# Kernel tuning notes

Hardware: AMD Instinct MI355X
Metric: run time of the kernel (lower is better)

## Reference

```python
import jax, jax.numpy as jnp
import numpy as np

B, S, HIDDEN = 4, 2048, 1024
HEADS = 16
D = HIDDEN // HEADS  # att_size = 64
SCALE = D ** -0.5


def setup_inputs() -> dict:
    key = jax.random.key(0)
    k_x, k_qkv, k_out = jax.random.split(key, 3)
    x = jax.random.normal(k_x, (B, S, HIDDEN), dtype=jnp.float32)
    # torch Linear weights: (out_features, in_features); xavier-uniform init
    lim_qkv = np.sqrt(6.0 / (HIDDEN + 3 * HIDDEN))
    W_qkv = jax.random.uniform(k_qkv, (3 * HEADS * D, HIDDEN), dtype=jnp.float32,
                               minval=-lim_qkv, maxval=lim_qkv)
    lim_out = np.sqrt(6.0 / (HIDDEN + HIDDEN))
    W_out = jax.random.uniform(k_out, (HIDDEN, HEADS * D), dtype=jnp.float32,
                               minval=-lim_out, maxval=lim_out)
    return {"x": x, "W_qkv": W_qkv, "W_out": W_out}


def reference(x, W_qkv, W_out):
    b, s, _ = x.shape
    # fused QKV projection; feature layout along output dim is [3][heads][d]
    qkv = jnp.einsum('bsh,fh->bsf', x, W_qkv).reshape(b, s, 3, HEADS, D)
    q = qkv[:, :, 0].transpose(0, 2, 1, 3) * SCALE  # [b, H, s, d]
    k = qkv[:, :, 1].transpose(0, 2, 1, 3)
    v = qkv[:, :, 2].transpose(0, 2, 1, 3)
    scores = jnp.einsum('bhqd,bhkd->bhqk', q, k)
    attn = jax.nn.softmax(scores, axis=-1)
    ctx = jnp.einsum('bhqk,bhkd->bhqd', attn, v)
    ctx = ctx.transpose(0, 2, 1, 3).reshape(b, s, HEADS * D)
    return jnp.einsum('bsf,hf->bsh', ctx, W_out)
```

## Files before the change

### kernel.cpp

```cpp
#include <hip/hip_runtime.h>
#include <hip/hip_bf16.h>
#include <stdint.h>
#include <math.h>


using half8  = __attribute__((ext_vector_type(8))) _Float16;
using half4  = __attribute__((ext_vector_type(4))) _Float16;
using f32x4  = __attribute__((ext_vector_type(4))) float;
using f32x16 = __attribute__((ext_vector_type(16))) float;
using u32x4  = __attribute__((ext_vector_type(4))) unsigned int;

#define HID   1024
#define NHEAD 16
#define HDIM  64
#define NB    4
#define SEQ   2048
#define MROWS (NB*SEQ)
#define NKTH  16

typedef __attribute__((address_space(1))) const void* gas_t;
typedef __attribute__((address_space(3))) void*       las_t;

__global__ void conv_h(const float* __restrict__ in, _Float16* __restrict__ out,
                       int n4, int nscale, float qs){
  int i = blockIdx.x * 256 + threadIdx.x;
  if (i >= n4) return;
  f32x4 v = *(const f32x4*)(in + (size_t)i*4);
  int row = (i*4) >> 10;
  if (row < nscale){ v[0]*=qs; v[1]*=qs; v[2]*=qs; v[3]*=qs; }
  half4 o = { (_Float16)v[0], (_Float16)v[1], (_Float16)v[2], (_Float16)v[3] };
  *(half4*)(out + (size_t)i*4) = o;
}

__device__ __forceinline__ void stage_tile(const _Float16* __restrict__ g,
                                           char* lds, int t, int wid){
#pragma unroll
  for (int i = 0; i < 4; ++i){
    int tl  = i*256 + t;
    int row = tl >> 3;
    int srcb = (((tl & 7) << 4)) ^ ((row & 7) << 4);
    __builtin_amdgcn_global_load_lds(
        (gas_t)((const char*)(g + (size_t)row*1024) + srcb),
        (las_t)(lds + (i*256 + wid*64)*16), 16, 0, 0);
  }
}

template<int EPI>
__global__ __launch_bounds__(256)
void gemmh(const _Float16* __restrict__ A, const _Float16* __restrict__ B,
           float* __restrict__ C,
           _Float16* __restrict__ qo, _Float16* __restrict__ ko,
           _Float16* __restrict__ vo, int N)
{
  __shared__ __align__(16) char lA[128*128];
  __shared__ __align__(16) char lB[128*128];
  int t = threadIdx.x, lane = t & 63, wid = t >> 6;
  int fq = lane >> 4, fr = lane & 15;
  int m0 = blockIdx.x * 128, n0 = blockIdx.y * 128;
  int wm = (wid >> 1) * 64, wn = (wid & 1) * 64;
  f32x4 acc[4][4] = {};

  for (int kt = 0; kt < NKTH; ++kt){
    stage_tile(A + (size_t)m0*1024 + kt*64, lA, t, wid);
    stage_tile(B + (size_t)n0*1024 + kt*64, lB, t, wid);
    __syncthreads();
#pragma unroll
    for (int kc = 0; kc < 2; ++kc){
      half8 af[4], bf[4];
#pragma unroll
      for (int mi = 0; mi < 4; ++mi){
        int row = wm + mi*16 + fr;
        af[mi] = *(const half8*)(lA + row*128 + ((kc*64 + fq*16) ^ ((row&7)<<4)));
      }
#pragma unroll
      for (int ni = 0; ni < 4; ++ni){
        int row = wn + ni*16 + fr;
        bf[ni] = *(const half8*)(lB + row*128 + ((kc*64 + fq*16) ^ ((row&7)<<4)));
      }
      __builtin_amdgcn_s_setprio(1);
#pragma unroll
      for (int mi = 0; mi < 4; ++mi)
#pragma unroll
        for (int ni = 0; ni < 4; ++ni)
          acc[mi][ni] = __builtin_amdgcn_mfma_f32_16x16x32_f16(af[mi], bf[ni],
                                                               acc[mi][ni], 0, 0, 0);
      __builtin_amdgcn_s_setprio(0);
    }
    __syncthreads();
  }

  if (EPI == 0){
#pragma unroll
    for (int mi = 0; mi < 4; ++mi)
#pragma unroll
      for (int ni = 0; ni < 4; ++ni)
#pragma unroll
        for (int r = 0; r < 4; ++r){
          int m = m0 + wm + mi*16 + fq*4 + r;
          int n = n0 + wn + ni*16 + fr;
          C[(size_t)m*N + n] = acc[mi][ni][r];
        }
  } else {
    int cls = n0 >> 10;
#pragma unroll
    for (int mi = 0; mi < 4; ++mi)
#pragma unroll
      for (int ni = 0; ni < 4; ++ni)
#pragma unroll
        for (int r = 0; r < 4; ++r){
          int m = m0 + wm + mi*16 + fq*4 + r;
          int n = n0 + wn + ni*16 + fr;
          float v = acc[mi][ni][r];
          int b = m >> 11, s = m & 2047;
          int nn = n & 1023;
          int h = nn >> 6, d2 = nn & 63;
          int bh = b*NHEAD + h;
          if (cls == 0){
            qo[((size_t)bh*SEQ + s)*HDIM + d2] = (_Float16)v;
          } else if (cls == 1){
            int kb = s >> 5, l31 = s & 31;
            int c = d2 >> 4, hi8 = (d2 >> 3) & 1, e = d2 & 7;
            ko[((((size_t)bh*64 + kb)*4 + c)*64 + hi8*32 + l31)*8 + e] = (_Float16)v;
          } else {
            int kb = s >> 5, kk = s & 31;
            int kh = kk >> 4, hv = (kk >> 3) & 1, e = kk & 7;
            int dh = d2 >> 5, lv = d2 & 31;
            vo[((((size_t)bh*64 + kb)*4 + dh*2 + kh)*64 + hv*32 + lv)*8 + e] = (_Float16)v;
          }
        }
  }
}

#define MFMA32H(A,B,C) __builtin_amdgcn_mfma_f32_32x32x16_f16(A, B, C, 0, 0, 0)

__device__ __forceinline__ void stage_kv(const char* Kg, const char* Vg, int kt,
                                         char* dK, char* dV, int t, int wid){
  const char* ks = Kg + (size_t)kt*8192;
  const char* vs = Vg + (size_t)kt*8192;
#pragma unroll
  for (int i = 0; i < 2; ++i){
    int sl = i*256 + t;
    __builtin_amdgcn_global_load_lds((gas_t)(ks + sl*16),
                                     (las_t)(dK + (i*256 + wid*64)*16), 16, 0, 0);
  }
#pragma unroll
  for (int i = 0; i < 2; ++i){
    int sl = i*256 + t;
    __builtin_amdgcn_global_load_lds((gas_t)(vs + sl*16),
                                     (las_t)(dV + (i*256 + wid*64)*16), 16, 0, 0);
  }
}

__global__ __launch_bounds__(256)
void attn_fused(const _Float16* __restrict__ Qs, const _Float16* __restrict__ KF,
                const _Float16* __restrict__ VF, _Float16* __restrict__ ctx)
{
  __shared__ __align__(16) char lK[2][8192];
  __shared__ __align__(16) char lV[2][8192];
  int t = threadIdx.x, lane = t & 63, wid = t >> 6;
  int l31 = lane & 31, hi8 = lane >> 5;

  int orig = blockIdx.x;
  int wg = (orig & 7) * 128 + (orig >> 3);
  int bh = wg >> 4, qt = wg & 15;

  const _Float16* Qb = Qs + (size_t)bh*SEQ*HDIM;
  const char* Kg = (const char*)(KF + (size_t)bh*64*4*64*8);
  const char* Vg = (const char*)(VF + (size_t)bh*64*4*64*8);
  int qg = qt*128 + wid*32 + l31;

  half8 qf[4];
#pragma unroll
  for (int c = 0; c < 4; ++c)
    qf[c] = *(const half8*)&Qb[(size_t)qg*HDIM + c*16 + hi8*8];

  f32x16 BIAS;
#pragma unroll
  for (int i = 0; i < 16; ++i) BIAS[i] = -4.0f;

  f32x16 av0 = {}, av1 = {};
  f32x4 lq = {};

  stage_kv(Kg, Vg, 0, lK[0], lV[0], t, wid);
  int cur = 0;

  for (int kt = 0; kt < 32; ++kt){
    asm volatile("s_waitcnt vmcnt(0)" ::: "memory");
    __builtin_amdgcn_s_barrier();
    if (kt + 1 < 32) stage_kv(Kg, Vg, kt + 1, lK[cur ^ 1], lV[cur ^ 1], t, wid);

#pragma unroll
    for (int st = 0; st < 2; ++st){
      const char* kp = lK[cur] + st*4096 + lane*16;
      const char* vp = lV[cur] + st*4096 + lane*16;
      half8 kf0 = *(const half8*)(kp);
      half8 kf1 = *(const half8*)(kp + 1024);
      half8 kf2 = *(const half8*)(kp + 2048);
      half8 kf3 = *(const half8*)(kp + 3072);
      half8 vf00 = *(const half8*)(vp);
      half8 vf01 = *(const half8*)(vp + 1024);
      half8 vf10 = *(const half8*)(vp + 2048);
      half8 vf11 = *(const half8*)(vp + 3072);

      __builtin_amdgcn_s_setprio(1);
      f32x16 sc = MFMA32H(kf0, qf[0], BIAS);
      sc = MFMA32H(kf1, qf[1], sc);
      sc = MFMA32H(kf2, qf[2], sc);
      sc = MFMA32H(kf3, qf[3], sc);
      __builtin_amdgcn_s_setprio(0);

#pragma unroll
      for (int i = 0; i < 16; ++i) sc[i] = __builtin_amdgcn_exp2f(sc[i]);
      lq[0] += (sc[0]+sc[1])   + (sc[2]+sc[3]);
      lq[1] += (sc[4]+sc[5])   + (sc[6]+sc[7]);
      lq[2] += (sc[8]+sc[9])   + (sc[10]+sc[11]);
      lq[3] += (sc[12]+sc[13]) + (sc[14]+sc[15]);

      uint32_t a0,a1,a2,a3,b0,b1,b2,b3;
      asm("v_cvt_pkrtz_f16_f32 %0, %1, %2" : "=v"(a0) : "v"(sc[0]),  "v"(sc[1]));
      asm("v_cvt_pkrtz_f16_f32 %0, %1, %2" : "=v"(a1) : "v"(sc[2]),  "v"(sc[3]));
      asm("v_cvt_pkrtz_f16_f32 %0, %1, %2" : "=v"(a2) : "v"(sc[4]),  "v"(sc[5]));
      asm("v_cvt_pkrtz_f16_f32 %0, %1, %2" : "=v"(a3) : "v"(sc[6]),  "v"(sc[7]));
      asm("v_cvt_pkrtz_f16_f32 %0, %1, %2" : "=v"(b0) : "v"(sc[8]),  "v"(sc[9]));
      asm("v_cvt_pkrtz_f16_f32 %0, %1, %2" : "=v"(b1) : "v"(sc[10]), "v"(sc[11]));
      asm("v_cvt_pkrtz_f16_f32 %0, %1, %2" : "=v"(b2) : "v"(sc[12]), "v"(sc[13]));
      asm("v_cvt_pkrtz_f16_f32 %0, %1, %2" : "=v"(b3) : "v"(sc[14]), "v"(sc[15]));
      asm volatile("v_permlane32_swap_b32 %0, %1" : "+v"(a0), "+v"(a2));
      asm volatile("v_permlane32_swap_b32 %0, %1" : "+v"(a1), "+v"(a3));
      asm volatile("v_permlane32_swap_b32 %0, %1" : "+v"(b0), "+v"(b2));
      asm volatile("v_permlane32_swap_b32 %0, %1" : "+v"(b1), "+v"(b3));
      u32x4 w0; w0.x=a0; w0.y=a1; w0.z=a2; w0.w=a3;
      u32x4 w1; w1.x=b0; w1.y=b1; w1.z=b2; w1.w=b3;
      half8 pf0 = __builtin_bit_cast(half8, w0);
      half8 pf1 = __builtin_bit_cast(half8, w1);

      __builtin_amdgcn_s_setprio(1);
      av0 = MFMA32H(vf00, pf0, av0);
      av0 = MFMA32H(vf01, pf1, av0);
      av1 = MFMA32H(vf10, pf0, av1);
      av1 = MFMA32H(vf11, pf1, av1);
      __builtin_amdgcn_s_setprio(0);
    }
    cur ^= 1;
  }

  float lh = (lq[0]+lq[1]) + (lq[2]+lq[3]);
  float lt = lh + __shfl_xor(lh, 32);
  float linv = 1.0f / lt;
  int b = bh >> 4, h = bh & 15;
  _Float16* orow = ctx + ((size_t)b*SEQ + qg)*HID + h*64;
#pragma unroll
  for (int g = 0; g < 4; ++g){
    half4 o0, o1;
#pragma unroll
    for (int i = 0; i < 4; ++i){
      o0[i] = (_Float16)(av0[g*4+i]*linv);
      o1[i] = (_Float16)(av1[g*4+i]*linv);
    }
    *(half4*)(orow + g*8 + hi8*4)      = o0;
    *(half4*)(orow + 32 + g*8 + hi8*4) = o1;
  }
}

extern "C" void kernel_launch(void* const* d_in, const int* in_sizes, int n_in,
                              void* d_out, int out_size, void* d_ws, size_t ws_size,
                              hipStream_t stream)
{
  const float* x  = (const float*)d_in[0];
  const float* Wq = (const float*)d_in[1];
  const float* Wo = (const float*)d_in[2];
  float* out = (float*)d_out;
  char* ws = (char*)d_ws;

  _Float16* XH  = (_Float16*)(ws);
  _Float16* WQH = (_Float16*)(ws + 16777216);
  _Float16* QH  = (_Float16*)(ws + 23068672);
  _Float16* KFb = (_Float16*)(ws + 39845888);
  _Float16* VFb = (_Float16*)(ws + 56623104);
  _Float16* CH  = (_Float16*)(ws + 73400320);
  _Float16* WOH = (_Float16*)(ws + 90177536);

  const float qs = 0.125f * 1.4426950408889634f;

  conv_h<<<(MROWS*HID/4)/256, 256, 0, stream>>>(x,  XH,  MROWS*HID/4, 0, 1.0f);
  conv_h<<<(3*HID*HID/4)/256, 256, 0, stream>>>(Wq, WQH, 3*HID*HID/4, HID, qs);
  conv_h<<<(HID*HID/4)/256, 256, 0, stream>>>(Wo, WOH, HID*HID/4, 0, 1.0f);

  gemmh<1><<<dim3(64, 24), 256, 0, stream>>>(XH, WQH, nullptr, QH, KFb, VFb, 3*HID);

  attn_fused<<<dim3(1024), 256, 0, stream>>>(QH, KFb, VFb, CH);

  gemmh<0><<<dim3(64, 8), 256, 0, stream>>>(CH, WOH, out, nullptr, nullptr, nullptr, HID);
}
```

Before: 206.5 us.

## Replace QKV GEMM with 256x256-tile double-buffered 8-wave pipelined kernel

Swaps the QKV projection GEMM for a new kernel with 256x256 output tiles, 512 threads, and double-buffered LDS. It overlaps async global-to-LDS loads of the next K slice with MFMA work on the current one, using explicit vmcnt/lgkmcnt waits and barriers. This aims to hide load latency and raise data reuse per tile compared with the single-buffered 128x128 kernel that synced on every K step. The grid drops to 384 blocks, which is close to one wave of blocks on the device. The hand-placed waits are fragile, and the large per-thread accumulator set adds register pressure.

New measurement: 218.0 us. 1.06x slower.

```diff
diff --git a/kernel.cpp b/kernel.cpp
--- a/kernel.cpp
+++ b/kernel.cpp
@@ -32,6 +32,126 @@
   *(half4*)(out + (size_t)i*4) = o;
 }
 
+#define BARR __builtin_amdgcn_s_barrier()
+#define LG0  asm volatile("s_waitcnt lgkmcnt(0)" ::: "memory")
+#define VM4  asm volatile("s_waitcnt vmcnt(4)" ::: "memory")
+#define VM0  asm volatile("s_waitcnt vmcnt(0)" ::: "memory")
+
+__device__ __forceinline__ void stage_half(const _Float16* __restrict__ G,
+                                           int r0, int c0, _Float16* dst, int t){
+#pragma unroll
+  for (int i = 0; i < 2; ++i){
+    int tl = i*512 + t;
+    int row = tl >> 3;
+    int col = ((tl & 7)*8) ^ ((row & 7) << 3);
+    __builtin_amdgcn_global_load_lds((gas_t)(G + (size_t)(r0+row)*1024 + c0 + col),
+                                     (las_t)(dst + (size_t)tl*8), 16, 0, 0);
+  }
+}
+
+#define SA(D,H,KT) do{ if((KT)<NKTH) stage_half(A, m0+(H)*128, (KT)*64, &As[D][H][0], t); }while(0)
+#define SB(D,H,KT) do{ if((KT)<NKTH) stage_half(B, n0+(H)*128, (KT)*64, &Bs[D][H][0], t); }while(0)
+
+#define RDA(D,MH) do{ _Pragma("unroll") for(int mi=0;mi<4;++mi){            \
+  int r = (MH)*64 + mi*16 + fr;                                             \
+  const char* p = (const char*)&As[D][wr][0] + r*128;                       \
+  af[mi][0] = *(const half8*)(p + ((     fq*16) ^ ((r&7)<<4)));             \
+  af[mi][1] = *(const half8*)(p + ((64 + fq*16) ^ ((r&7)<<4))); }}while(0)
+
+#define RDB(D,NH,BS) do{ _Pragma("unroll") for(int ni=0;ni<2;++ni){         \
+  int r = (wc&1)*64 + (NH)*32 + ni*16 + fr;                                 \
+  const char* p = (const char*)&Bs[D][wc>>1][0] + r*128;                    \
+  BS[ni][0] = *(const half8*)(p + ((     fq*16) ^ ((r&7)<<4)));             \
+  BS[ni][1] = *(const half8*)(p + ((64 + fq*16) ^ ((r&7)<<4))); }}while(0)
+
+#define MM(MH,NH,BS) do{ __builtin_amdgcn_s_setprio(1);                     \
+  _Pragma("unroll") for(int mi=0;mi<4;++mi)                                 \
+  _Pragma("unroll") for(int ni=0;ni<2;++ni){                                \
+    acc[(MH)*4+mi][(NH)*2+ni] = __builtin_amdgcn_mfma_f32_16x16x32_f16(     \
+        af[mi][0], BS[ni][0], acc[(MH)*4+mi][(NH)*2+ni], 0, 0, 0);          \
+    acc[(MH)*4+mi][(NH)*2+ni] = __builtin_amdgcn_mfma_f32_16x16x32_f16(     \
+        af[mi][1], BS[ni][1], acc[(MH)*4+mi][(NH)*2+ni], 0, 0, 0); }        \
+  __builtin_amdgcn_s_setprio(0); }while(0)
+
+__global__ __launch_bounds__(512, 2)
+void gemm256(const _Float16* __restrict__ A, const _Float16* __restrict__ B,
+             _Float16* __restrict__ qo, _Float16* __restrict__ ko,
+             _Float16* __restrict__ vo)
+{
+  __shared__ __align__(16) _Float16 As[2][2][8192];
+  __shared__ __align__(16) _Float16 Bs[2][2][8192];
+  int t = threadIdx.x, lane = t & 63, wid = t >> 6;
+  int fq = lane >> 4, fr = lane & 15;
+  int wr = wid >> 2, wc = wid & 3;
+  int m0 = blockIdx.x * 256, n0 = blockIdx.y * 256;
+
+  f32x4 acc[8][4] = {};
+  half8 af[4][2], bs0[2][2], bs1[2][2];
+
+  SA(0,0,0); SA(0,1,0); SB(0,0,0); SB(0,1,0);
+  SB(1,0,1); SB(1,1,1);
+  VM4; BARR;
+
+  for (int j = 0; j < NKTH/2; ++j){
+    int T = 2*j;
+    bool last = (j == NKTH/2 - 1);
+    RDA(0,0); RDB(0,0,bs0);
+    SA(1,0,T+1);
+    BARR; LG0; MM(0,0,bs0); BARR;
+    RDB(0,1,bs1);
+    SA(1,1,T+1);
+    BARR; LG0; MM(0,1,bs1); BARR;
+    RDA(0,1);
+    SB(0,0,T+2);
+    BARR; LG0; MM(1,0,bs0); BARR;
+    SB(0,1,T+2);
+    BARR; MM(1,1,bs1);
+    if (last) { VM0; } else { VM4; }
+    BARR;
+    RDA(1,0); RDB(1,0,bs0);
+    SA(0,0,T+2);
+    BARR; LG0; MM(0,0,bs0); BARR;
+    RDB(1,1,bs1);
+    SA(0,1,T+2);
+    BARR; LG0; MM(0,1,bs1); BARR;
+    RDA(1,1);
+    SB(1,0,T+3);
+    BARR; LG0; MM(1,0,bs0); BARR;
+    SB(1,1,T+3);
+    BARR; MM(1,1,bs1);
+    if (!last) { VM4; }
+    BARR;
+  }
+
+  int cls = n0 >> 10;
+#pragma unroll
+  for (int mi = 0; mi < 8; ++mi)
+#pragma unroll
+    for (int ni = 0; ni < 4; ++ni)
+#pragma unroll
+      for (int r = 0; r < 4; ++r){
+        int m = m0 + wr*128 + mi*16 + fq*4 + r;
+        int n = n0 + wc*64 + ni*16 + fr;
+        float v = acc[mi][ni][r];
+        int b = m >> 11, s = m & 2047;
+        int nn = n & 1023;
+        int h = nn >> 6, d2 = nn & 63;
+        int bh = b*NHEAD + h;
+        if (cls == 0){
+          qo[((size_t)bh*SEQ + s)*HDIM + d2] = (_Float16)v;
+        } else if (cls == 1){
+          int kb = s >> 5, l31 = s & 31;
+          int c = d2 >> 4, hi8 = (d2 >> 3) & 1, e = d2 & 7;
+          ko[((((size_t)bh*64 + kb)*4 + c)*64 + hi8*32 + l31)*8 + e] = (_Float16)v;
+        } else {
+          int kb = s >> 5, kk = s & 31;
+          int kh = kk >> 4, hv = (kk >> 3) & 1, e = kk & 7;
+          int dh = d2 >> 5, lv = d2 & 31;
+          vo[((((size_t)bh*64 + kb)*4 + dh*2 + kh)*64 + hv*32 + lv)*8 + e] = (_Float16)v;
+        }
+      }
+}
+
 __device__ __forceinline__ void stage_tile(const _Float16* __restrict__ g,
                                            char* lds, int t, int wid){
 #pragma unroll
@@ -45,12 +165,9 @@
   }
 }
 
-template<int EPI>
 __global__ __launch_bounds__(256)
-void gemmh(const _Float16* __restrict__ A, const _Float16* __restrict__ B,
-           float* __restrict__ C,
-           _Float16* __restrict__ qo, _Float16* __restrict__ ko,
-           _Float16* __restrict__ vo, int N)
+void gemmo(const _Float16* __restrict__ A, const _Float16* __restrict__ B,
+           float* __restrict__ C, int N)
 {
   __shared__ __align__(16) char lA[128*128];
   __shared__ __align__(16) char lB[128*128];
@@ -89,46 +206,16 @@
     __syncthreads();
   }
 
-  if (EPI == 0){
-#pragma unroll
-    for (int mi = 0; mi < 4; ++mi)
-#pragma unroll
-      for (int ni = 0; ni < 4; ++ni)
-#pragma unroll
-        for (int r = 0; r < 4; ++r){
-          int m = m0 + wm + mi*16 + fq*4 + r;
-          int n = n0 + wn + ni*16 + fr;
-          C[(size_t)m*N + n] = acc[mi][ni][r];
-        }
-  } else {
-    int cls = n0 >> 10;
-#pragma unroll
-    for (int mi = 0; mi < 4; ++mi)
-#pragma unroll
-      for (int ni = 0; ni < 4; ++ni)
-#pragma unroll
-        for (int r = 0; r < 4; ++r){
-          int m = m0 + wm + mi*16 + fq*4 + r;
-          int n = n0 + wn + ni*16 + fr;
-          float v = acc[mi][ni][r];
-          int b = m >> 11, s = m & 2047;
-          int nn = n & 1023;
-          int h = nn >> 6, d2 = nn & 63;
-          int bh = b*NHEAD + h;
-          if (cls == 0){
-            qo[((size_t)bh*SEQ + s)*HDIM + d2] = (_Float16)v;
-          } else if (cls == 1){
-            int kb = s >> 5, l31 = s & 31;
-            int c = d2 >> 4, hi8 = (d2 >> 3) & 1, e = d2 & 7;
-            ko[((((size_t)bh*64 + kb)*4 + c)*64 + hi8*32 + l31)*8 + e] = (_Float16)v;
-          } else {
-            int kb = s >> 5, kk = s & 31;
-            int kh = kk >> 4, hv = (kk >> 3) & 1, e = kk & 7;
-            int dh = d2 >> 5, lv = d2 & 31;
-            vo[((((size_t)bh*64 + kb)*4 + dh*2 + kh)*64 + hv*32 + lv)*8 + e] = (_Float16)v;
-          }
-        }
-  }
+#pragma unroll
+  for (int mi = 0; mi < 4; ++mi)
+#pragma unroll
+    for (int ni = 0; ni < 4; ++ni)
+#pragma unroll
+      for (int r = 0; r < 4; ++r){
+        int m = m0 + wm + mi*16 + fq*4 + r;
+        int n = n0 + wn + ni*16 + fr;
+        C[(size_t)m*N + n] = acc[mi][ni][r];
+      }
 }
 
 #define MFMA32H(A,B,C) __builtin_amdgcn_mfma_f32_32x32x16_f16(A, B, C, 0, 0, 0)
@@ -286,9 +373,9 @@
   conv_h<<<(3*HID*HID/4)/256, 256, 0, stream>>>(Wq, WQH, 3*HID*HID/4, HID, qs);
   conv_h<<<(HID*HID/4)/256, 256, 0, stream>>>(Wo, WOH, HID*HID/4, 0, 1.0f);
 
-  gemmh<1><<<dim3(64, 24), 256, 0, stream>>>(XH, WQH, nullptr, QH, KFb, VFb, 3*HID);
+  gemm256<<<dim3(32, 12), 512, 0, stream>>>(XH, WQH, QH, KFb, VFb);
 
   attn_fused<<<dim3(1024), 256, 0, stream>>>(QH, KFb, VFb, CH);
 
-  gemmh<0><<<dim3(64, 8), 256, 0, stream>>>(CH, WOH, out, nullptr, nullptr, nullptr, HID);
-}
+  gemmo<<<dim3(64, 8), 256, 0, stream>>>(CH, WOH, out, HID);
+}
```
